# Kernel optimization log

Hardware: AMD Instinct MI355X
Metric: run time of the kernel (lower is better)

The kernel has to match this reference:

```python
import jax, jax.numpy as jnp
import numpy as np

N = 100000
E = 1600000
F_IN, H, C = 128, 128, 64


def setup_inputs() -> dict:
    key = jax.random.key(0)
    ks = jax.random.split(key, 8)
    x = jax.random.normal(ks[0], (N, F_IN), dtype=jnp.float32)
    edge_index = jax.random.randint(ks[1], (2, E), 0, N, dtype=jnp.int64)
    s = lambda fi: (1.0 / np.sqrt(fi))
    # SAGEConv1: lin_l (applied to mean-aggregated neighbors, has bias), lin_r (root, no bias)
    W1l = jax.random.uniform(ks[2], (H, F_IN), jnp.float32, -s(F_IN), s(F_IN))
    b1 = jnp.zeros((H,), jnp.float32)
    W1r = jax.random.uniform(ks[3], (H, F_IN), jnp.float32, -s(F_IN), s(F_IN))
    # SAGEConv2
    W2l = jax.random.uniform(ks[4], (C, H), jnp.float32, -s(H), s(H))
    b2 = jnp.zeros((C,), jnp.float32)
    W2r = jax.random.uniform(ks[5], (C, H), jnp.float32, -s(H), s(H))
    return {"x": x, "edge_index": edge_index, "W1l": W1l, "b1": b1, "W1r": W1r,
            "W2l": W2l, "b2": b2, "W2r": W2r}


def _mean_aggr(x, src, dst):
    # mean over incoming neighbors (PyG flow: edge_index[0]=source -> edge_index[1]=target)
    msg = x[src]                                            # [E, F] big gather
    summed = jax.ops.segment_sum(msg, dst, num_segments=N)  # [N, F]
    cnt = jax.ops.segment_sum(jnp.ones((src.shape[0],), x.dtype), dst, num_segments=N)
    return summed / jnp.clip(cnt, 1.0)[:, None]


def _sage_conv(x, src, dst, Wl, b, Wr):
    agg = _mean_aggr(x, src, dst)
    return agg @ Wl.T + b + x @ Wr.T


def _iconv(x, src, dst):
    # weight-free GCN propagation: D^-1/2 (A + I) D^-1/2 @ x
    loops = jnp.arange(N, dtype=src.dtype)
    s2 = jnp.concatenate([src, loops])
    d2 = jnp.concatenate([dst, loops])
    deg = jax.ops.segment_sum(jnp.ones((s2.shape[0],), x.dtype), d2, num_segments=N)
    dis = jnp.where(deg > 0, jax.lax.rsqrt(jnp.maximum(deg, 1.0)), 0.0)
    norm = dis[s2] * dis[d2]                               # [E+N]
    return jax.ops.segment_sum(norm[:, None] * x[s2], d2, num_segments=N)


def reference(x, edge_index, W1l, b1, W1r, W2l, b2, W2r):
    src, dst = edge_index[0], edge_index[1]
    h = jax.nn.relu(_sage_conv(x, src, dst, W1l, b1, W1r))
    # F.dropout(training=False) -> identity in eval mode
    h = _sage_conv(h, src, dst, W2l, b2, W2r)
    return _iconv(h, src, dst)
```

## Files before the change

### kernel.cpp

```cpp
#include <hip/hip_runtime.h>

#define GN 100000
#define GE 1600000
#define GF 128
#define GH 128
#define GC 64

#define NB 392
#define SLABSZ 5376
#define P1_EDGES 4096
#define P1_BLOCKS ((GE + P1_EDGES - 1) / P1_EDGES)
#define CASTX_BLOCKS 12500

typedef __attribute__((ext_vector_type(8))) short v8s;
typedef __attribute__((ext_vector_type(4))) float v4f;
typedef __attribute__((ext_vector_type(2))) float v2f;

__device__ __forceinline__ unsigned short f2bf(float f) {
    union { float f; unsigned u; } a; a.f = f;
    unsigned r = a.u + 0x7fff + ((a.u >> 16) & 1);
    return (unsigned short)(r >> 16);
}
__device__ __forceinline__ float bf2f(unsigned short b) {
    union { unsigned u; float f; } a; a.u = ((unsigned)b) << 16;
    return a.f;
}
__device__ __forceinline__ v2f cvt2(unsigned w) {
    union { unsigned u; float f; } lo, hi;
    lo.u = w << 16; hi.u = w & 0xffff0000u;
    return (v2f){lo.f, hi.f};
}

__global__ __launch_bounds__(256) void prep_kernel(
    unsigned* __restrict__ slab, int* __restrict__ bucket_cnt,
    const int* __restrict__ src, const int* __restrict__ dst,
    unsigned short* __restrict__ xb, const float* __restrict__ x,
    unsigned short* w1l, unsigned short* w1r,
    unsigned short* w2l, unsigned short* w2r,
    const float* W1l, const float* W1r,
    const float* W2l, const float* W2r)
{
    __shared__ int hist[512];
    __shared__ int scanex[512];
    __shared__ int cursor[512];
    __shared__ int gbase[512];
    __shared__ int ssum[256];
    __shared__ unsigned stage[P1_EDGES];
    __shared__ unsigned short sbid[P1_EDGES];

    int tid = threadIdx.x;
    int blk = blockIdx.x;

    if (blk >= P1_BLOCKS) {
        int cb = blk - P1_BLOCKS;
        if (cb < CASTX_BLOCKS) {
            int i = cb * 256 + tid;
            float4 v = ((const float4*)x)[i];
            ushort4 u;
            u.x = f2bf(v.x); u.y = f2bf(v.y); u.z = f2bf(v.z); u.w = f2bf(v.w);
            ((ushort4*)xb)[i] = u;
            return;
        }
        int i = (cb - CASTX_BLOCKS) * 256 + tid;
        const float* s; unsigned short* d; int off;
        if      (i <  4096) { s = W1l; d = w1l; off = i; }
        else if (i <  8192) { s = W1r; d = w1r; off = i - 4096; }
        else if (i < 10240) { s = W2l; d = w2l; off = i - 8192; }
        else if (i < 12288) { s = W2r; d = w2r; off = i - 10240; }
        else return;
        float4 v = ((const float4*)s)[off];
        ushort4 u;
        u.x = f2bf(v.x); u.y = f2bf(v.y); u.z = f2bf(v.z); u.w = f2bf(v.w);
        ((ushort4*)d)[off] = u;
        return;
    }

    int e0 = blk * P1_EDGES;
    int nE = min(P1_EDGES, GE - e0);

    unsigned pk[16]; int bk[16];
    hist[tid] = 0; hist[tid + 256] = 0;
    __syncthreads();
    #pragma unroll
    for (int j = 0; j < 16; ++j) {
        int i = j * 256 + tid;
        if (i < nE) {
            int e = e0 + i;
            int d = dst[e], s = src[e];
            int b = d >> 8;
            pk[j] = ((unsigned)(d & 255) << 17) | (unsigned)s;
            bk[j] = b;
            atomicAdd(&hist[b], 1);
        } else bk[j] = -1;
    }
    __syncthreads();
    int a0 = hist[2 * tid], a1 = hist[2 * tid + 1];
    int s2 = a0 + a1;
    ssum[tid] = s2;
    __syncthreads();
    for (int off = 1; off < 256; off <<= 1) {
        int v = (tid >= off) ? ssum[tid - off] : 0;
        __syncthreads();
        ssum[tid] += v;
        __syncthreads();
    }
    int pbase = ssum[tid] - s2;
    scanex[2 * tid] = pbase;          cursor[2 * tid] = pbase;
    scanex[2 * tid + 1] = pbase + a0; cursor[2 * tid + 1] = pbase + a0;
    __syncthreads();
    #pragma unroll
    for (int j = 0; j < 16; ++j) {
        if (bk[j] >= 0) {
            int pos = atomicAdd(&cursor[bk[j]], 1);
            stage[pos] = pk[j];
            sbid[pos] = (unsigned short)bk[j];
        }
    }
    for (int b = tid; b < NB; b += 256) {
        int c = hist[b];
        gbase[b] = c ? atomicAdd(&bucket_cnt[b], c) : 0;
    }
    __syncthreads();
    for (int i = tid; i < nE; i += 256) {
        int b = sbid[i];
        int go = gbase[b] + (i - scanex[b]);
        if (go < SLABSZ)
            slab[(size_t)b * SLABSZ + go] = stage[i];
    }
}

__global__ __launch_bounds__(256) void bucket_pass2_kernel(
    int* __restrict__ csr, int* __restrict__ row_ptr,
    float* __restrict__ invc, float* __restrict__ dis,
    const unsigned* __restrict__ slab, const int* __restrict__ bucket_cnt)
{
    __shared__ int deg_l[256];
    __shared__ int excl[256];
    __shared__ int cur[256];
    __shared__ int ssum[256];
    __shared__ int bstart_s;
    __shared__ unsigned stage[SLABSZ];

    int t = threadIdx.x;
    int b = blockIdx.x;

    int c0 = (2 * t < NB) ? bucket_cnt[2 * t] : 0;
    int c1 = (2 * t + 1 < NB) ? bucket_cnt[2 * t + 1] : 0;
    int sc = c0 + c1;
    ssum[t] = sc;
    __syncthreads();
    for (int off = 1; off < 256; off <<= 1) {
        int v = (t >= off) ? ssum[t - off] : 0;
        __syncthreads();
        ssum[t] += v;
        __syncthreads();
    }
    int pb = ssum[t] - sc;
    if (2 * t == b)     bstart_s = pb;
    if (2 * t + 1 == b) bstart_s = pb + c0;
    if (b == NB - 1 && t == 0) row_ptr[GN] = GE;

    int cnt = min(bucket_cnt[b], SLABSZ);
    const unsigned* sp = slab + (size_t)b * SLABSZ;
    deg_l[t] = 0;
    __syncthreads();
    int base = bstart_s;
    for (int i = t; i < cnt; i += 256)
        atomicAdd(&deg_l[sp[i] >> 17], 1);
    __syncthreads();
    int dg = deg_l[t];
    ssum[t] = dg;
    __syncthreads();
    for (int off = 1; off < 256; off <<= 1) {
        int v = (t >= off) ? ssum[t - off] : 0;
        __syncthreads();
        ssum[t] += v;
        __syncthreads();
    }
    int ex = ssum[t] - dg;
    excl[t] = ex; cur[t] = ex;
    __syncthreads();
    int d = b * 256 + t;
    if (d < GN) {
        row_ptr[d] = base + ex;
        float c = (float)dg;
        invc[d] = 1.0f / fmaxf(c, 1.0f);
        dis[d] = rsqrtf(c + 1.0f);
    }
    for (int i = t; i < cnt; i += 256) {
        unsigned p = sp[i];
        int pos = atomicAdd(&cur[p >> 17], 1);
        stage[pos] = p & 0x1FFFFu;
    }
    __syncthreads();
    for (int i = t; i < cnt; i += 256)
        csr[base + i] = (int)stage[i];
}

__global__ __launch_bounds__(64, 3) void sage1_fused_kernel(
    unsigned short* __restrict__ P, unsigned short* __restrict__ Q,
    const unsigned short* __restrict__ xb,
    const unsigned short* __restrict__ W1, const unsigned short* __restrict__ W2,
    const unsigned short* __restrict__ Wl, const unsigned short* __restrict__ Wr,
    const float* __restrict__ b1, const float* __restrict__ b2,
    const float* __restrict__ invc, const int* __restrict__ row_ptr,
    const int* __restrict__ csr)
{
    __shared__ unsigned short hsA[16][136];
    __shared__ unsigned short hsB[16][136];

    int lane = threadIdx.x;
    int lm = lane & 15, quad = lane >> 4;
    int m_base = blockIdx.x * 16;

    int rp = row_ptr[m_base + min(lane, 16)];
    float icv = invc[m_base + lm];

    for (int r = 0; r < 16; ++r) {
        int beg = __builtin_amdgcn_readlane(rp, r);
        int end = __builtin_amdgcn_readlane(rp, r + 1);
        int d = end - beg;
        float a0 = 0.f, a1 = 0.f;
        if (d > 0) {
            int dc = min(d, 64);
            int idx = csr[beg + ((lane < dc) ? lane : (dc - 1))];
            for (int t = 0; t < dc; t += 16) {
                unsigned v[16];
                #pragma unroll
                for (int u = 0; u < 16; ++u) {
                    int tt = t + u;
                    int s = __builtin_amdgcn_readlane(idx, (tt < dc) ? tt : (dc - 1));
                    unsigned x = ((const unsigned*)(xb + (size_t)s * 128))[lane];
                    v[u] = (tt < dc) ? x : 0u;
                }
                #pragma unroll
                for (int u = 0; u < 16; ++u) {
                    a0 += bf2f((unsigned short)(v[u] & 0xffff));
                    a1 += bf2f((unsigned short)(v[u] >> 16));
                }
            }
            for (int j = beg + 64; j < end; ++j) {
                int s = __builtin_amdgcn_readfirstlane(csr[j]);
                unsigned x = ((const unsigned*)(xb + (size_t)s * 128))[lane];
                a0 += bf2f((unsigned short)(x & 0xffff));
                a1 += bf2f((unsigned short)(x >> 16));
            }
        }
        float ic = __int_as_float(__builtin_amdgcn_readlane(__float_as_int(icv), r));
        unsigned w = (unsigned)f2bf(a0 * ic) | ((unsigned)f2bf(a1 * ic) << 16);
        *(unsigned*)&hsA[r][2 * lane] = w;
    }

    v4f acc[8];
    #pragma unroll
    for (int nt = 0; nt < 8; ++nt) acc[nt] = (v4f){0.f,0.f,0.f,0.f};

    #pragma unroll
    for (int ks = 0; ks < 4; ++ks) {
        int koff = ks * 32 + quad * 8;
        v8s a1f = *(const v8s*)&hsA[lm][koff];
        v8s a2f = *(const v8s*)(xb + (size_t)(m_base + lm) * 128 + koff);
        #pragma unroll
        for (int nt = 0; nt < 8; ++nt) {
            int col = nt * 16 + lm;
            v8s w1 = *(const v8s*)(W1 + (size_t)col * 128 + koff);
            v8s w2 = *(const v8s*)(W2 + (size_t)col * 128 + koff);
            acc[nt] = __builtin_amdgcn_mfma_f32_16x16x32_bf16(a1f, w1, acc[nt], 0, 0, 0);
            acc[nt] = __builtin_amdgcn_mfma_f32_16x16x32_bf16(a2f, w2, acc[nt], 0, 0, 0);
        }
    }

    #pragma unroll
    for (int nt = 0; nt < 8; ++nt) {
        int col = nt * 16 + lm;
        float bv = b1[col];
        #pragma unroll
        for (int r = 0; r < 4; ++r) {
            int rl = quad * 4 + r;
            hsB[rl][col] = f2bf(fmaxf(acc[nt][r] + bv, 0.f));
        }
    }

    v4f accP[4], accQ[4];
    #pragma unroll
    for (int nt = 0; nt < 4; ++nt) {
        accP[nt] = (v4f){0.f,0.f,0.f,0.f};
        accQ[nt] = (v4f){0.f,0.f,0.f,0.f};
    }

    #pragma unroll
    for (int ks = 0; ks < 4; ++ks) {
        int koff = ks * 32 + quad * 8;
        v8s af = *(const v8s*)&hsB[lm][koff];
        #pragma unroll
        for (int nt = 0; nt < 4; ++nt) {
            int col = nt * 16 + lm;
            v8s bl = *(const v8s*)(Wl + (size_t)col * 128 + koff);
            v8s br = *(const v8s*)(Wr + (size_t)col * 128 + koff);
            accP[nt] = __builtin_amdgcn_mfma_f32_16x16x32_bf16(af, bl, accP[nt], 0, 0, 0);
            accQ[nt] = __builtin_amdgcn_mfma_f32_16x16x32_bf16(af, br, accQ[nt], 0, 0, 0);
        }
    }

    #pragma unroll
    for (int nt = 0; nt < 4; ++nt) {
        int col = nt * 16 + lm;
        float b2v = b2[col];
        #pragma unroll
        for (int r = 0; r < 4; ++r) {
            int row = m_base + quad * 4 + r;
            P[(size_t)row * 64 + col] = f2bf(accP[nt][r]);
            Q[(size_t)row * 64 + col] = f2bf(accQ[nt][r] + b2v);
        }
    }
}

__global__ __launch_bounds__(256) void gather_combine_kernel(
    unsigned short* __restrict__ h2s, const unsigned short* __restrict__ p,
    const unsigned short* __restrict__ q,
    const float* __restrict__ invc, const float* __restrict__ dis,
    const int* __restrict__ row_ptr, const int* __restrict__ csr, int N)
{
    int wid = (blockIdx.x * 256 + threadIdx.x) >> 6;
    int lane = threadIdx.x & 63;
    if (wid >= N) return;
    int beg = __builtin_amdgcn_readfirstlane(row_ptr[wid]);
    int end = __builtin_amdgcn_readfirstlane(row_ptr[wid + 1]);
    int d = end - beg;
    int grp = lane >> 3, lx = lane & 7;
    v2f a0 = {0.f,0.f}, a1 = {0.f,0.f}, a2 = {0.f,0.f}, a3 = {0.f,0.f};

    int nf = d >> 3;
    #pragma unroll 2
    for (int t = 0; t < nf; ++t) {
        int j = beg + t * 8;
        int s0 = csr[j],     s1 = csr[j + 1], s2 = csr[j + 2], s3 = csr[j + 3];
        int s4 = csr[j + 4], s5 = csr[j + 5], s6 = csr[j + 6], s7 = csr[j + 7];
        int t0 = (lane & 8) ? s1 : s0; int t1 = (lane & 8) ? s3 : s2;
        int t2 = (lane & 8) ? s5 : s4; int t3 = (lane & 8) ? s7 : s6;
        int u0 = (lane & 16) ? t1 : t0; int u1 = (lane & 16) ? t3 : t2;
        int ss = (lane & 32) ? u1 : u0;
        uint4 v = ((const uint4*)(p + (size_t)ss * 64))[lx];
        a0 += cvt2(v.x); a1 += cvt2(v.y); a2 += cvt2(v.z); a3 += cvt2(v.w);
    }
    int rem = d & 7;
    if (rem) {
        int j = beg + nf * 8;
        int rc = rem - 1;
        int s0 = csr[j];
        int s1 = csr[j + min(1, rc)]; int s2 = csr[j + min(2, rc)];
        int s3 = csr[j + min(3, rc)]; int s4 = csr[j + min(4, rc)];
        int s5 = csr[j + min(5, rc)]; int s6 = csr[j + min(6, rc)];
        int s7 = csr[j + min(7, rc)];
        int t0 = (lane & 8) ? s1 : s0; int t1 = (lane & 8) ? s3 : s2;
        int t2 = (lane & 8) ? s5 : s4; int t3 = (lane & 8) ? s7 : s6;
        int u0 = (lane & 16) ? t1 : t0; int u1 = (lane & 16) ? t3 : t2;
        int ss = (lane & 32) ? u1 : u0;
        uint4 v = ((const uint4*)(p + (size_t)ss * 64))[lx];
        bool ok = grp < rem;
        v.x = ok ? v.x : 0u; v.y = ok ? v.y : 0u;
        v.z = ok ? v.z : 0u; v.w = ok ? v.w : 0u;
        a0 += cvt2(v.x); a1 += cvt2(v.y); a2 += cvt2(v.z); a3 += cvt2(v.w);
    }
    #pragma unroll
    for (int m = 8; m <= 32; m <<= 1) {
        a0.x += __shfl_xor(a0.x, m); a0.y += __shfl_xor(a0.y, m);
        a1.x += __shfl_xor(a1.x, m); a1.y += __shfl_xor(a1.y, m);
        a2.x += __shfl_xor(a2.x, m); a2.y += __shfl_xor(a2.y, m);
        a3.x += __shfl_xor(a3.x, m); a3.y += __shfl_xor(a3.y, m);
    }
    if (grp == 0) {
        float ic = invc[wid], dd = dis[wid];
        uint4 qv = ((const uint4*)(q + (size_t)wid * 64))[lx];
        v2f q0 = cvt2(qv.x), q1 = cvt2(qv.y), q2 = cvt2(qv.z), q3 = cvt2(qv.w);
        uint4 o;
        o.x = (unsigned)f2bf(dd * (a0.x * ic + q0.x)) | ((unsigned)f2bf(dd * (a0.y * ic + q0.y)) << 16);
        o.y = (unsigned)f2bf(dd * (a1.x * ic + q1.x)) | ((unsigned)f2bf(dd * (a1.y * ic + q1.y)) << 16);
        o.z = (unsigned)f2bf(dd * (a2.x * ic + q2.x)) | ((unsigned)f2bf(dd * (a2.y * ic + q2.y)) << 16);
        o.w = (unsigned)f2bf(dd * (a3.x * ic + q3.x)) | ((unsigned)f2bf(dd * (a3.y * ic + q3.y)) << 16);
        ((uint4*)(h2s + (size_t)wid * 64))[lx] = o;
    }
}

__global__ __launch_bounds__(256) void iconv_kernel(
    float* __restrict__ out, const unsigned short* __restrict__ h2s,
    const float* __restrict__ dis, const int* __restrict__ row_ptr,
    const int* __restrict__ csr, int N)
{
    int wid = (blockIdx.x * 256 + threadIdx.x) >> 6;
    int lane = threadIdx.x & 63;
    if (wid >= N) return;
    int beg = __builtin_amdgcn_readfirstlane(row_ptr[wid]);
    int end = __builtin_amdgcn_readfirstlane(row_ptr[wid + 1]);
    int d = end - beg;
    int grp = lane >> 3, lx = lane & 7;
    v2f a0 = {0.f,0.f}, a1 = {0.f,0.f}, a2 = {0.f,0.f}, a3 = {0.f,0.f};

    int nf = d >> 3;
    #pragma unroll 2
    for (int t = 0; t < nf; ++t) {
        int j = beg + t * 8;
        int s0 = csr[j],     s1 = csr[j + 1], s2 = csr[j + 2], s3 = csr[j + 3];
        int s4 = csr[j + 4], s5 = csr[j + 5], s6 = csr[j + 6], s7 = csr[j + 7];
        int t0 = (lane & 8) ? s1 : s0; int t1 = (lane & 8) ? s3 : s2;
        int t2 = (lane & 8) ? s5 : s4; int t3 = (lane & 8) ? s7 : s6;
        int u0 = (lane & 16) ? t1 : t0; int u1 = (lane & 16) ? t3 : t2;
        int ss = (lane & 32) ? u1 : u0;
        uint4 v = ((const uint4*)(h2s + (size_t)ss * 64))[lx];
        a0 += cvt2(v.x); a1 += cvt2(v.y); a2 += cvt2(v.z); a3 += cvt2(v.w);
    }
    int rem = d & 7;
    if (rem) {
        int j = beg + nf * 8;
        int rc = rem - 1;
        int s0 = csr[j];
        int s1 = csr[j + min(1, rc)]; int s2 = csr[j + min(2, rc)];
        int s3 = csr[j + min(3, rc)]; int s4 = csr[j + min(4, rc)];
        int s5 = csr[j + min(5, rc)]; int s6 = csr[j + min(6, rc)];
        int s7 = csr[j + min(7, rc)];
        int t0 = (lane & 8) ? s1 : s0; int t1 = (lane & 8) ? s3 : s2;
        int t2 = (lane & 8) ? s5 : s4; int t3 = (lane & 8) ? s7 : s6;
        int u0 = (lane & 16) ? t1 : t0; int u1 = (lane & 16) ? t3 : t2;
        int ss = (lane & 32) ? u1 : u0;
        uint4 v = ((const uint4*)(h2s + (size_t)ss * 64))[lx];
        bool ok = grp < rem;
        v.x = ok ? v.x : 0u; v.y = ok ? v.y : 0u;
        v.z = ok ? v.z : 0u; v.w = ok ? v.w : 0u;
        a0 += cvt2(v.x); a1 += cvt2(v.y); a2 += cvt2(v.z); a3 += cvt2(v.w);
    }
    #pragma unroll
    for (int m = 8; m <= 32; m <<= 1) {
        a0.x += __shfl_xor(a0.x, m); a0.y += __shfl_xor(a0.y, m);
        a1.x += __shfl_xor(a1.x, m); a1.y += __shfl_xor(a1.y, m);
        a2.x += __shfl_xor(a2.x, m); a2.y += __shfl_xor(a2.y, m);
        a3.x += __shfl_xor(a3.x, m); a3.y += __shfl_xor(a3.y, m);
    }
    if (grp == 0) {
        uint4 sv = ((const uint4*)(h2s + (size_t)wid * 64))[lx];
        v2f s0 = cvt2(sv.x), s1 = cvt2(sv.y), s2 = cvt2(sv.z), s3 = cvt2(sv.w);
        float dd = dis[wid];
        float4 o0 = make_float4(dd * (a0.x + s0.x), dd * (a0.y + s0.y),
                                dd * (a1.x + s1.x), dd * (a1.y + s1.y));
        float4 o1 = make_float4(dd * (a2.x + s2.x), dd * (a2.y + s2.y),
                                dd * (a3.x + s3.x), dd * (a3.y + s3.y));
        ((float4*)(out + (size_t)wid * 64))[lx * 2]     = o0;
        ((float4*)(out + (size_t)wid * 64))[lx * 2 + 1] = o1;
    }
}

extern "C" void kernel_launch(void* const* d_in, const int* in_sizes, int n_in,
                              void* d_out, int out_size, void* d_ws, size_t ws_size,
                              hipStream_t stream) {
    const float* x   = (const float*)d_in[0];
    const int*   ei  = (const int*)d_in[1];
    const float* W1l = (const float*)d_in[2];
    const float* b1  = (const float*)d_in[3];
    const float* W1r = (const float*)d_in[4];
    const float* W2l = (const float*)d_in[5];
    const float* b2  = (const float*)d_in[6];
    const float* W2r = (const float*)d_in[7];
    float* out = (float*)d_out;

    const int* src = ei;
    const int* dst = ei + GE;

    float* invc = (float*)d_ws;
    float* dis  = invc + GN;
    unsigned short* regA = (unsigned short*)(dis + GN);
    unsigned short* regB = regA + (size_t)GN * 128;
    unsigned short* xb    = regA;
    unsigned short* w1lb = regB + (size_t)GN * 128;
    unsigned short* w1rb = w1lb + GH * GF;
    unsigned short* w2lb = w1rb + GH * GF;
    unsigned short* w2rb = w2lb + GC * GH;
    int* row_ptr      = (int*)(w2rb + GC * GH);
    int* bucket_cnt   = row_ptr + GN + 1;
    unsigned* slab    = (unsigned*)(bucket_cnt + NB);
    int* csr          = (int*)(slab + (size_t)NB * SLABSZ);
    unsigned short* pq = (unsigned short*)(csr + GE);
    unsigned short* pb = pq;
    unsigned short* qb = pq + (size_t)GN * 64;
    unsigned short* h2s = regB;

    const int T = 256;
    const int g_wave = (GN * 64 + T - 1) / T;

    hipMemsetAsync(bucket_cnt, 0, NB * sizeof(int), stream);
    prep_kernel<<<P1_BLOCKS + CASTX_BLOCKS + 48, T, 0, stream>>>(
        slab, bucket_cnt, src, dst,
        xb, x, w1lb, w1rb, w2lb, w2rb, W1l, W1r, W2l, W2r);

    bucket_pass2_kernel<<<NB, T, 0, stream>>>(csr, row_ptr, invc, dis,
                                              slab, bucket_cnt);

    sage1_fused_kernel<<<GN / 16, 64, 0, stream>>>(pb, qb, xb,
                                                   w1lb, w1rb, w2lb, w2rb,
                                                   b1, b2, invc, row_ptr, csr);

    gather_combine_kernel<<<g_wave, T, 0, stream>>>(h2s, pb, qb, invc, dis,
                                                    row_ptr, csr, GN);

    iconv_kernel<<<g_wave, T, 0, stream>>>(out, h2s, dis, row_ptr, csr, GN);
}
```

Before: 359.6 us.

## Split fused SAGE kernel across four waves per 16-row tile

The fused SAGE layer-1 kernel now runs 256 threads (4 waves) per 16-row tile instead of a single wave. Each wave gathers and averages neighbor features for 4 of the 16 rows, then computes its own slice of the output columns in both MFMA stages, with __syncthreads between stages. This spreads the serial per-row gather latency and the MFMA work over more waves to raise parallelism and latency hiding. In exchange it adds block-level barriers and reduces per-wave work granularity.

```diff
diff --git a/kernel.cpp b/kernel.cpp
--- a/kernel.cpp
+++ b/kernel.cpp
@@ -197,7 +197,7 @@
         csr[base + i] = (int)stage[i];
 }
 
-__global__ __launch_bounds__(64, 3) void sage1_fused_kernel(
+__global__ __launch_bounds__(256, 4) void sage_fused_kernel(
     unsigned short* __restrict__ P, unsigned short* __restrict__ Q,
     const unsigned short* __restrict__ xb,
     const unsigned short* __restrict__ W1, const unsigned short* __restrict__ W2,
@@ -209,16 +209,16 @@
     __shared__ unsigned short hsA[16][136];
     __shared__ unsigned short hsB[16][136];
 
-    int lane = threadIdx.x;
+    int tid = threadIdx.x;
+    int wv = tid >> 6, lane = tid & 63;
     int lm = lane & 15, quad = lane >> 4;
     int m_base = blockIdx.x * 16;
 
-    int rp = row_ptr[m_base + min(lane, 16)];
-    float icv = invc[m_base + lm];
-
-    for (int r = 0; r < 16; ++r) {
-        int beg = __builtin_amdgcn_readlane(rp, r);
-        int end = __builtin_amdgcn_readlane(rp, r + 1);
+    for (int rr = 0; rr < 4; ++rr) {
+        int rloc = wv * 4 + rr;
+        int row = m_base + rloc;
+        int beg = __builtin_amdgcn_readfirstlane(row_ptr[row]);
+        int end = __builtin_amdgcn_readfirstlane(row_ptr[row + 1]);
         int d = end - beg;
         float a0 = 0.f, a1 = 0.f;
         if (d > 0) {
@@ -246,14 +246,15 @@
                 a1 += bf2f((unsigned short)(x >> 16));
             }
         }
-        float ic = __int_as_float(__builtin_amdgcn_readlane(__float_as_int(icv), r));
+        float ic = invc[row];
         unsigned w = (unsigned)f2bf(a0 * ic) | ((unsigned)f2bf(a1 * ic) << 16);
-        *(unsigned*)&hsA[r][2 * lane] = w;
-    }
-
-    v4f acc[8];
-    #pragma unroll
-    for (int nt = 0; nt < 8; ++nt) acc[nt] = (v4f){0.f,0.f,0.f,0.f};
+        *(unsigned*)&hsA[rloc][2 * lane] = w;
+    }
+    __syncthreads();
+
+    v4f acc[2];
+    acc[0] = (v4f){0.f,0.f,0.f,0.f};
+    acc[1] = (v4f){0.f,0.f,0.f,0.f};
 
     #pragma unroll
     for (int ks = 0; ks < 4; ++ks) {
@@ -261,8 +262,8 @@
         v8s a1f = *(const v8s*)&hsA[lm][koff];
         v8s a2f = *(const v8s*)(xb + (size_t)(m_base + lm) * 128 + koff);
         #pragma unroll
-        for (int nt = 0; nt < 8; ++nt) {
-            int col = nt * 16 + lm;
+        for (int nt = 0; nt < 2; ++nt) {
+            int col = wv * 32 + nt * 16 + lm;
             v8s w1 = *(const v8s*)(W1 + (size_t)col * 128 + koff);
             v8s w2 = *(const v8s*)(W2 + (size_t)col * 128 + koff);
             acc[nt] = __builtin_amdgcn_mfma_f32_16x16x32_bf16(a1f, w1, acc[nt], 0, 0, 0);
@@ -271,47 +272,35 @@
     }
 
     #pragma unroll
-    for (int nt = 0; nt < 8; ++nt) {
-        int col = nt * 16 + lm;
+    for (int nt = 0; nt < 2; ++nt) {
+        int col = wv * 32 + nt * 16 + lm;
         float bv = b1[col];
         #pragma unroll
-        for (int r = 0; r < 4; ++r) {
-            int rl = quad * 4 + r;
-            hsB[rl][col] = f2bf(fmaxf(acc[nt][r] + bv, 0.f));
-        }
-    }
-
-    v4f accP[4], accQ[4];
-    #pragma unroll
-    for (int nt = 0; nt < 4; ++nt) {
-        accP[nt] = (v4f){0.f,0.f,0.f,0.f};
-        accQ[nt] = (v4f){0.f,0.f,0.f,0.f};
-    }
+        for (int r = 0; r < 4; ++r)
+            hsB[quad * 4 + r][col] = f2bf(fmaxf(acc[nt][r] + bv, 0.f));
+    }
+    __syncthreads();
+
+    v4f accP = (v4f){0.f,0.f,0.f,0.f};
+    v4f accQ = (v4f){0.f,0.f,0.f,0.f};
+    int col = wv * 16 + lm;
 
     #pragma unroll
     for (int ks = 0; ks < 4; ++ks) {
         int koff = ks * 32 + quad * 8;
         v8s af = *(const v8s*)&hsB[lm][koff];
-        #pragma unroll
-        for (int nt = 0; nt < 4; ++nt) {
-            int col = nt * 16 + lm;
-            v8s bl = *(const v8s*)(Wl + (size_t)col * 128 + koff);
-            v8s br = *(const v8s*)(Wr + (size_t)col * 128 + koff);
-            accP[nt] = __builtin_amdgcn_mfma_f32_16x16x32_bf16(af, bl, accP[nt], 0, 0, 0);
-            accQ[nt] = __builtin_amdgcn_mfma_f32_16x16x32_bf16(af, br, accQ[nt], 0, 0, 0);
-        }
-    }
-
-    #pragma unroll
-    for (int nt = 0; nt < 4; ++nt) {
-        int col = nt * 16 + lm;
-        float b2v = b2[col];
-        #pragma unroll
-        for (int r = 0; r < 4; ++r) {
-            int row = m_base + quad * 4 + r;
-            P[(size_t)row * 64 + col] = f2bf(accP[nt][r]);
-            Q[(size_t)row * 64 + col] = f2bf(accQ[nt][r] + b2v);
-        }
+        v8s bl = *(const v8s*)(Wl + (size_t)col * 128 + koff);
+        v8s br = *(const v8s*)(Wr + (size_t)col * 128 + koff);
+        accP = __builtin_amdgcn_mfma_f32_16x16x32_bf16(af, bl, accP, 0, 0, 0);
+        accQ = __builtin_amdgcn_mfma_f32_16x16x32_bf16(af, br, accQ, 0, 0, 0);
+    }
+
+    float b2v = b2[col];
+    #pragma unroll
+    for (int r = 0; r < 4; ++r) {
+        int row = m_base + quad * 4 + r;
+        P[(size_t)row * 64 + col] = f2bf(accP[r]);
+        Q[(size_t)row * 64 + col] = f2bf(accQ[r] + b2v);
     }
 }
 
@@ -493,9 +482,9 @@
     bucket_pass2_kernel<<<NB, T, 0, stream>>>(csr, row_ptr, invc, dis,
                                               slab, bucket_cnt);
 
-    sage1_fused_kernel<<<GN / 16, 64, 0, stream>>>(pb, qb, xb,
-                                                   w1lb, w1rb, w2lb, w2rb,
-                                                   b1, b2, invc, row_ptr, csr);
+    sage_fused_kernel<<<GN / 16, T, 0, stream>>>(pb, qb, xb,
+                                                 w1lb, w1rb, w2lb, w2rb,
+                                                 b1, b2, invc, row_ptr, csr);
 
     gather_combine_kernel<<<g_wave, T, 0, stream>>>(h2s, pb, qb, invc, dis,
                                                     row_ptr, csr, GN);
```

New measurement: 363.8 us. Within noise of the previous version (+1.2%).
